# Kernel tuning notes

Hardware: AMD Instinct MI355X
Metric: run time of the kernel (lower is better)

Reference implementation:

```python
import jax, jax.numpy as jnp
import numpy as np

B, C, H, W = 8, 64, 32, 32
NEG = 256
TEMP = 2.0
FACTOR = 0.8
EPS = 1e-8


def setup_inputs() -> dict:
    key = jax.random.key(0)
    k1, k2, k3, k4 = jax.random.split(key, 4)
    views_1 = jax.random.normal(k1, (B, C, H, W), dtype=jnp.float32)
    views_2 = jax.random.normal(k2, (B, C, H, W), dtype=jnp.float32)
    img = jax.random.uniform(k3, (1, 3, H, W), dtype=jnp.float32)
    neg_idx = jax.random.randint(k4, (B, 2, H * W, NEG), 0, H, dtype=jnp.int32)
    return {"views_1": views_1, "views_2": views_2, "img": img, "neg_idx": neg_idx}


def _forward(views_1, views_2, img, neg_idx):
    hw = H * W
    height = jnp.arange(hw) // W
    width = jnp.arange(hw) % W
    coords = jnp.stack([height, width]).astype(jnp.float32)  # [2, hw]
    img0 = img[0]  # [3, H, W]; original uses img[0] for EVERY batch element
    euc_norm = jnp.sqrt(jnp.asarray((H - 1) ** 2 + (W - 1) ** 2, jnp.float32))
    sqrt3 = jnp.sqrt(jnp.asarray(3.0, jnp.float32))

    center = img0[:, height, width]  # [3, hw]

    def per_sample(z1, z2, nidx):
        # nidx: [2, hw, neg]
        nf = nidx.astype(jnp.float32)
        # torch.norm with no dim => scalar Frobenius norm over [2, neg] per pixel
        d = coords[:, :, None] - nf  # [2, hw, neg]
        euc = jnp.sqrt(jnp.sum(d * d, axis=(0, 2))) / euc_norm  # [hw]
        negs = img0[:, nidx[0], nidx[1]]  # [3, hw, neg]
        rd = center[:, :, None] - negs
        rgb = jnp.sqrt(jnp.sum(rd * rd, axis=(0, 2))) / sqrt3  # [hw]
        weight = euc * FACTOR + rgb * (1.0 - FACTOR)  # [hw], constant across neg

        z1v = z1.reshape(C, hw)  # [c, hw]
        pn = z2[:, nidx[0], nidx[1]]  # [c, hw, neg]
        dot = jnp.einsum('cp,cpn->pn', z1v, pn)  # [hw, neg]
        z1sq = jnp.sum(z1v * z1v, axis=0)  # [hw]
        z1n = jnp.sqrt(z1sq)
        pnn = jnp.sqrt(jnp.sum(pn * pn, axis=0))  # [hw, neg]
        cos = dot / jnp.maximum(z1n[:, None] * pnn, EPS)  # [hw, neg]
        cos0 = z1sq / jnp.maximum(z1sq, EPS)  # [hw] (self-similarity ~ 1)

        sim_neg = jnp.minimum(jnp.abs(cos * weight[:, None]), 1.0)  # [hw, neg]
        sim0 = jnp.minimum(jnp.abs(cos0), 1.0)  # [hw]
        sim = jnp.concatenate(
            [jnp.mean(sim0)[None], jnp.mean(sim_neg, axis=0) / TEMP]
        )  # [neg+1]

        # BCELoss with target = [1, 0, ..., 0]; torch clamps log terms at -100
        logp = jnp.maximum(jnp.log(sim[0]), -100.0)
        log1m = jnp.maximum(jnp.log1p(-sim[1:]), -100.0)
        bce = -(logp + jnp.sum(log1m)) / (NEG + 1)
        return bce, sim

    bce, sims = jax.vmap(per_sample)(views_1, views_2, neg_idx)
    loss = jnp.mean(bce)
    sim_all = jnp.sum(sims, axis=0)
    return (loss, sim_all[0] / B, jnp.sum(sim_all[1:]) / NEG * TEMP / B)


def reference(views_1, views_2, img, neg_idx):
    return _forward(views_1, views_2, img, neg_idx)
```

## Files before the change

kernel.cpp:

```cpp
#include <hip/hip_runtime.h>
#include <math.h>

#define BB 8
#define CC 64
#define HH 32
#define WW 32
#define HW 1024
#define NEGN 256
#define TEMP 2.0f
#define FACTOR 0.8f
#define EPSF 1e-8f
#define PT 8


__global__ __launch_bounds__(256) void prep(
    const float* __restrict__ z1,
    const float* __restrict__ img,
    float* __restrict__ accSim,
    float* __restrict__ accSim0,
    float* __restrict__ z1n_ws,
    float4* __restrict__ imgpack)
{
    const int b = blockIdx.x;
    const int t = threadIdx.x;

    accSim[b * NEGN + t] = 0.f;

    if (t < HW / BB) {
        const int q = b * (HW / BB) + t;
        imgpack[q] = make_float4(img[q], img[HW + q], img[2 * HW + q], 0.f);
    }

    const float4* __restrict__ z1b =
        reinterpret_cast<const float4*>(z1 + (size_t)b * CC * HW);
    float4 s = make_float4(0.f, 0.f, 0.f, 0.f);
    #pragma unroll 8
    for (int c = 0; c < CC; ++c) {
        const float4 v = z1b[c * (HW / 4) + t];
        s.x = fmaf(v.x, v.x, s.x);
        s.y = fmaf(v.y, v.y, s.y);
        s.z = fmaf(v.z, v.z, s.z);
        s.w = fmaf(v.w, v.w, s.w);
    }
    reinterpret_cast<float4*>(z1n_ws + (size_t)b * HW)[t] =
        make_float4(sqrtf(s.x), sqrtf(s.y), sqrtf(s.z), sqrtf(s.w));

    float s0 = fminf(fabsf(s.x / fmaxf(s.x, EPSF)), 1.0f)
             + fminf(fabsf(s.y / fmaxf(s.y, EPSF)), 1.0f)
             + fminf(fabsf(s.z / fmaxf(s.z, EPSF)), 1.0f)
             + fminf(fabsf(s.w / fmaxf(s.w, EPSF)), 1.0f);
    #pragma unroll
    for (int off = 32; off; off >>= 1) s0 += __shfl_down(s0, off);
    __shared__ float red[4];
    if ((t & 63) == 0) red[t >> 6] = s0;
    __syncthreads();
    if (t == 0) accSim0[b] = red[0] + red[1] + red[2] + red[3];
}

__global__ __launch_bounds__(256, 4) void contrastive_fused(
    const float* __restrict__ z1,
    const float* __restrict__ z2,
    const int*   __restrict__ nidx,
    const float* __restrict__ z1n_ws,
    const float4* __restrict__ imgpack,
    float* __restrict__ accSim)
{
    __shared__ float Dt_s[PT * HW];

    const int t  = threadIdx.x;
    const int b  = blockIdx.x >> 7;
    const int p0 = (blockIdx.x & 127) * PT;

    const int lane32 = t & 31;
    const int pp_b   = t >> 5;
    const int p_b    = p0 + pp_b;

    const float4* __restrict__ z2f4 =
        reinterpret_cast<const float4*>(z2 + (size_t)b * CC * HW);
    const float* __restrict__ z1row = z1 + (size_t)(b * CC) * HW + p0;

    float4 acc[PT];
    #pragma unroll
    for (int pp = 0; pp < PT; ++pp) acc[pp] = make_float4(0.f, 0.f, 0.f, 0.f);
    float4 sq = make_float4(0.f, 0.f, 0.f, 0.f);

    float4 pf[4];
    #pragma unroll
    for (int i = 0; i < 4; ++i) pf[i] = z2f4[i * (HW / 4) + t];

#define GEMM_STEP(kk, bv)                                                      \
    {                                                                          \
        sq.x = fmaf((bv).x, (bv).x, sq.x);                                     \
        sq.y = fmaf((bv).y, (bv).y, sq.y);                                     \
        sq.z = fmaf((bv).z, (bv).z, sq.z);                                     \
        sq.w = fmaf((bv).w, (bv).w, sq.w);                                     \
        _Pragma("unroll")                                                      \
        for (int pp = 0; pp < PT; ++pp) {                                      \
            const float a = z1row[(kk) * HW + pp];      \
            acc[pp].x = fmaf(a, (bv).x, acc[pp].x);                            \
            acc[pp].y = fmaf(a, (bv).y, acc[pp].y);                            \
            acc[pp].z = fmaf(a, (bv).z, acc[pp].z);                            \
            acc[pp].w = fmaf(a, (bv).w, acc[pp].w);                            \
        }                                                                      \
    }

    #pragma unroll 4
    for (int k = 0; k < CC - 4; ++k) {
        const float4 bv = pf[k & 3];
        pf[k & 3] = z2f4[(k + 4) * (HW / 4) + t];
        GEMM_STEP(k, bv);
    }
    #pragma unroll
    for (int k = CC - 4; k < CC; ++k) {
        const float4 bv = pf[k & 3];
        GEMM_STEP(k, bv);
    }
#undef GEMM_STEP

    const float* __restrict__ z1nrow = z1n_ws + (size_t)b * HW + p0;
    float z1nv[PT];
    #pragma unroll
    for (int pp = 0; pp < PT; ++pp) z1nv[pp] = z1nrow[pp];
    const float4 pnn = make_float4(sqrtf(sq.x), sqrtf(sq.y),
                                   sqrtf(sq.z), sqrtf(sq.w));
    float4* Dt4 = reinterpret_cast<float4*>(Dt_s);
    #pragma unroll
    for (int pp = 0; pp < PT; ++pp) {
        float4 cv;
        cv.x = acc[pp].x / fmaxf(z1nv[pp] * pnn.x, EPSF);
        cv.y = acc[pp].y / fmaxf(z1nv[pp] * pnn.y, EPSF);
        cv.z = acc[pp].z / fmaxf(z1nv[pp] * pnn.z, EPSF);
        cv.w = acc[pp].w / fmaxf(z1nv[pp] * pnn.w, EPSF);
        Dt4[pp * (HW / 4) + t] = cv;
    }

    const size_t nbase = ((size_t)(b * 2) * HW + p_b) * NEGN;
    const int2* __restrict__ nr = reinterpret_cast<const int2*>(nidx + nbase);
    const int2* __restrict__ nc =
        reinterpret_cast<const int2*>(nidx + nbase + (size_t)HW * NEGN);
    int2 rrv[4], ccv[4];
    #pragma unroll
    for (int j = 0; j < 4; ++j) {
        rrv[j] = nr[lane32 + 32 * j];
        ccv[j] = nc[lane32 + 32 * j];
    }
    __syncthreads();

    const float4 cen = imgpack[p_b];
    const float hp = (float)(p_b >> 5), wp = (float)(p_b & 31);

    int q[8];
    #pragma unroll
    for (int j = 0; j < 4; ++j) {
        q[2 * j]     = rrv[j].x * WW + ccv[j].x;
        q[2 * j + 1] = rrv[j].y * WW + ccv[j].y;
    }
    float4 g[8];
    #pragma unroll
    for (int e = 0; e < 8; ++e) g[e] = imgpack[q[e]];
    float cg[8];
    #pragma unroll
    for (int e = 0; e < 8; ++e) cg[e] = Dt_s[pp_b * HW + q[e]];

    float se = 0.f, sr = 0.f;
    #pragma unroll
    for (int j = 0; j < 4; ++j) {
        {
            const float dh = hp - (float)rrv[j].x, dw = wp - (float)ccv[j].x;
            se += dh * dh + dw * dw;
            const float d0 = cen.x - g[2 * j].x;
            const float d1 = cen.y - g[2 * j].y;
            const float d2 = cen.z - g[2 * j].z;
            sr += d0 * d0 + d1 * d1 + d2 * d2;
        }
        {
            const float dh = hp - (float)rrv[j].y, dw = wp - (float)ccv[j].y;
            se += dh * dh + dw * dw;
            const float d0 = cen.x - g[2 * j + 1].x;
            const float d1 = cen.y - g[2 * j + 1].y;
            const float d2 = cen.z - g[2 * j + 1].z;
            sr += d0 * d0 + d1 * d1 + d2 * d2;
        }
    }
    #pragma unroll
    for (int off = 16; off; off >>= 1) {
        se += __shfl_xor(se, off);
        sr += __shfl_xor(sr, off);
    }
    const float euc_norm = sqrtf((float)((HH - 1) * (HH - 1) + (WW - 1) * (WW - 1)));
    const float weight = sqrtf(se) / euc_norm * FACTOR +
                         sqrtf(sr) / sqrtf(3.0f) * (1.0f - FACTOR);

    float2 sv[4];
    #pragma unroll
    for (int j = 0; j < 4; ++j) {
        sv[j].x = fminf(fabsf(cg[2 * j]     * weight), 1.0f);
        sv[j].y = fminf(fabsf(cg[2 * j + 1] * weight), 1.0f);
    }

    __syncthreads();
    float2* simpart2 = reinterpret_cast<float2*>(Dt_s);
    #pragma unroll
    for (int j = 0; j < 4; ++j)
        simpart2[pp_b * (NEGN / 2) + lane32 + 32 * j] = sv[j];
    __syncthreads();

    float s = 0.f;
    #pragma unroll
    for (int pp = 0; pp < PT; ++pp) s += Dt_s[pp * NEGN + t];
    atomicAdd(accSim + b * NEGN + t, s);
}

__global__ __launch_bounds__(256) void finalize(
    const float* __restrict__ accSim,
    const float* __restrict__ accSim0,
    float* __restrict__ out)
{
    const int t = threadIdx.x;
    float ssum = 0.f, lsum = 0.f;
    #pragma unroll
    for (int b = 0; b < BB; ++b) {
        const float s = accSim[b * NEGN + t] * (1.0f / HW) * (1.0f / TEMP);
        ssum += s;
        lsum += fmaxf(log1pf(-s), -100.0f);
    }
    __shared__ float rs[4], rl[4];
    #pragma unroll
    for (int off = 32; off; off >>= 1) {
        ssum += __shfl_down(ssum, off);
        lsum += __shfl_down(lsum, off);
    }
    if ((t & 63) == 0) { rs[t >> 6] = ssum; rl[t >> 6] = lsum; }
    __syncthreads();

    if (t == 0) {
        const float S = rs[0] + rs[1] + rs[2] + rs[3];
        const float L = rl[0] + rl[1] + rl[2] + rl[3];
        float logpsum = 0.f, sim0sum = 0.f;
        #pragma unroll
        for (int b = 0; b < BB; ++b) {
            const float s0 = accSim0[b] * (1.0f / HW);
            sim0sum += s0;
            logpsum += fmaxf(logf(s0), -100.0f);
        }
        out[0] = -(logpsum + L) / ((float)(NEGN + 1) * (float)BB);
        out[1] = sim0sum / (float)BB;
        out[2] = S / (float)NEGN * TEMP / (float)BB;
    }
}

extern "C" void kernel_launch(void* const* d_in, const int* in_sizes, int n_in,
                              void* d_out, int out_size, void* d_ws, size_t ws_size,
                              hipStream_t stream) {
    const float* v1   = (const float*)d_in[0];
    const float* v2   = (const float*)d_in[1];
    const float* img  = (const float*)d_in[2];
    const int*   nidx = (const int*)  d_in[3];

    float* ws      = (float*)d_ws;
    float* accSim  = ws;
    float* accSim0 = accSim + BB * NEGN;
    float* z1n_ws  = accSim0 + BB;
    float4* imgpack = (float4*)(z1n_ws + BB * HW);

    prep<<<BB, 256, 0, stream>>>(v1, img, accSim, accSim0, z1n_ws, imgpack);
    contrastive_fused<<<BB * (HW / PT), 256, 0, stream>>>(
        v1, v2, nidx, z1n_ws, imgpack, accSim);
    finalize<<<1, 256, 0, stream>>>(accSim, accSim0, (float*)d_out);
}
```

Baseline: 101.1 us.

## Fold prep kernel into main kernel and replace atomics with partial-sum buffer

```diff
diff --git a/kernel.cpp b/kernel.cpp
--- a/kernel.cpp
+++ b/kernel.cpp
@@ -11,82 +11,65 @@
 #define FACTOR 0.8f
 #define EPSF 1e-8f
 #define PT 8
-
-
-__global__ __launch_bounds__(256) void prep(
-    const float* __restrict__ z1,
-    const float* __restrict__ img,
-    float* __restrict__ accSim,
-    float* __restrict__ accSim0,
-    float* __restrict__ z1n_ws,
-    float4* __restrict__ imgpack)
-{
-    const int b = blockIdx.x;
-    const int t = threadIdx.x;
-
-    accSim[b * NEGN + t] = 0.f;
-
-    if (t < HW / BB) {
-        const int q = b * (HW / BB) + t;
-        imgpack[q] = make_float4(img[q], img[HW + q], img[2 * HW + q], 0.f);
-    }
-
-    const float4* __restrict__ z1b =
-        reinterpret_cast<const float4*>(z1 + (size_t)b * CC * HW);
-    float4 s = make_float4(0.f, 0.f, 0.f, 0.f);
-    #pragma unroll 8
-    for (int c = 0; c < CC; ++c) {
-        const float4 v = z1b[c * (HW / 4) + t];
-        s.x = fmaf(v.x, v.x, s.x);
-        s.y = fmaf(v.y, v.y, s.y);
-        s.z = fmaf(v.z, v.z, s.z);
-        s.w = fmaf(v.w, v.w, s.w);
-    }
-    reinterpret_cast<float4*>(z1n_ws + (size_t)b * HW)[t] =
-        make_float4(sqrtf(s.x), sqrtf(s.y), sqrtf(s.z), sqrtf(s.w));
-
-    float s0 = fminf(fabsf(s.x / fmaxf(s.x, EPSF)), 1.0f)
-             + fminf(fabsf(s.y / fmaxf(s.y, EPSF)), 1.0f)
-             + fminf(fabsf(s.z / fmaxf(s.z, EPSF)), 1.0f)
-             + fminf(fabsf(s.w / fmaxf(s.w, EPSF)), 1.0f);
-    #pragma unroll
-    for (int off = 32; off; off >>= 1) s0 += __shfl_down(s0, off);
-    __shared__ float red[4];
-    if ((t & 63) == 0) red[t >> 6] = s0;
-    __syncthreads();
-    if (t == 0) accSim0[b] = red[0] + red[1] + red[2] + red[3];
-}
+#define RING 8
+
 
 __global__ __launch_bounds__(256, 4) void contrastive_fused(
     const float* __restrict__ z1,
     const float* __restrict__ z2,
+    const float* __restrict__ img,
     const int*   __restrict__ nidx,
-    const float* __restrict__ z1n_ws,
-    const float4* __restrict__ imgpack,
-    float* __restrict__ accSim)
+    float* __restrict__ simPart,
+    float* __restrict__ sim0Part)
 {
+    __shared__ float As_s[CC * PT];
     __shared__ float Dt_s[PT * HW];
-
-    const int t  = threadIdx.x;
-    const int b  = blockIdx.x >> 7;
-    const int p0 = (blockIdx.x & 127) * PT;
+    __shared__ float z1n_s[PT];
+    __shared__ float z1sq_s[PT];
+
+    const int t   = threadIdx.x;
+    const int blk = blockIdx.x;
+    const int b   = blk >> 7;
+    const int p0  = (blk & 127) * PT;
 
     const int lane32 = t & 31;
     const int pp_b   = t >> 5;
     const int p_b    = p0 + pp_b;
 
+    for (int i = t; i < CC * PT; i += 256) {
+        const int c = i >> 3, pp = i & 7;
+        As_s[i] = z1[((size_t)(b * CC + c)) * HW + p0 + pp];
+    }
+    __syncthreads();
+
+    {
+        const int pp = t & 7;
+        float s = 0.f;
+        #pragma unroll
+        for (int c = 0; c < CC; ++c) { const float v = As_s[c * PT + pp]; s += v * v; }
+        if (t < PT) { z1sq_s[t] = s; z1n_s[t] = sqrtf(s); }
+    }
+    __syncthreads();
+
+    if (t == 0) {
+        float s0 = 0.f;
+        #pragma unroll
+        for (int pp = 0; pp < PT; ++pp)
+            s0 += fminf(fabsf(z1sq_s[pp] / fmaxf(z1sq_s[pp], EPSF)), 1.0f);
+        sim0Part[blk] = s0;
+    }
+
     const float4* __restrict__ z2f4 =
         reinterpret_cast<const float4*>(z2 + (size_t)b * CC * HW);
-    const float* __restrict__ z1row = z1 + (size_t)(b * CC) * HW + p0;
 
     float4 acc[PT];
     #pragma unroll
     for (int pp = 0; pp < PT; ++pp) acc[pp] = make_float4(0.f, 0.f, 0.f, 0.f);
     float4 sq = make_float4(0.f, 0.f, 0.f, 0.f);
 
-    float4 pf[4];
-    #pragma unroll
-    for (int i = 0; i < 4; ++i) pf[i] = z2f4[i * (HW / 4) + t];
+    float4 pf[RING];
+    #pragma unroll
+    for (int i = 0; i < RING; ++i) pf[i] = z2f4[i * (HW / 4) + t];
 
 #define GEMM_STEP(kk, bv)                                                      \
     {                                                                          \
@@ -94,33 +77,35 @@
         sq.y = fmaf((bv).y, (bv).y, sq.y);                                     \
         sq.z = fmaf((bv).z, (bv).z, sq.z);                                     \
         sq.w = fmaf((bv).w, (bv).w, sq.w);                                     \
+        const float4 a03 = reinterpret_cast<const float4*>(As_s)[(kk) * 2];    \
+        const float4 a47 = reinterpret_cast<const float4*>(As_s)[(kk) * 2 + 1];\
+        const float av[8] = {a03.x, a03.y, a03.z, a03.w,                       \
+                             a47.x, a47.y, a47.z, a47.w};                      \
         _Pragma("unroll")                                                      \
         for (int pp = 0; pp < PT; ++pp) {                                      \
-            const float a = z1row[(kk) * HW + pp];      \
-            acc[pp].x = fmaf(a, (bv).x, acc[pp].x);                            \
-            acc[pp].y = fmaf(a, (bv).y, acc[pp].y);                            \
-            acc[pp].z = fmaf(a, (bv).z, acc[pp].z);                            \
-            acc[pp].w = fmaf(a, (bv).w, acc[pp].w);                            \
+            acc[pp].x = fmaf(av[pp], (bv).x, acc[pp].x);                       \
+            acc[pp].y = fmaf(av[pp], (bv).y, acc[pp].y);                       \
+            acc[pp].z = fmaf(av[pp], (bv).z, acc[pp].z);                       \
+            acc[pp].w = fmaf(av[pp], (bv).w, acc[pp].w);                       \
         }                                                                      \
     }
 
-    #pragma unroll 4
-    for (int k = 0; k < CC - 4; ++k) {
-        const float4 bv = pf[k & 3];
-        pf[k & 3] = z2f4[(k + 4) * (HW / 4) + t];
+    #pragma unroll 8
+    for (int k = 0; k < CC - RING; ++k) {
+        const float4 bv = pf[k & (RING - 1)];
+        pf[k & (RING - 1)] = z2f4[(k + RING) * (HW / 4) + t];
         GEMM_STEP(k, bv);
     }
     #pragma unroll
-    for (int k = CC - 4; k < CC; ++k) {
-        const float4 bv = pf[k & 3];
+    for (int k = CC - RING; k < CC; ++k) {
+        const float4 bv = pf[k & (RING - 1)];
         GEMM_STEP(k, bv);
     }
 #undef GEMM_STEP
 
-    const float* __restrict__ z1nrow = z1n_ws + (size_t)b * HW + p0;
     float z1nv[PT];
     #pragma unroll
-    for (int pp = 0; pp < PT; ++pp) z1nv[pp] = z1nrow[pp];
+    for (int pp = 0; pp < PT; ++pp) z1nv[pp] = z1n_s[pp];
     const float4 pnn = make_float4(sqrtf(sq.x), sqrtf(sq.y),
                                    sqrtf(sq.z), sqrtf(sq.w));
     float4* Dt4 = reinterpret_cast<float4*>(Dt_s);
@@ -146,7 +131,7 @@
     }
     __syncthreads();
 
-    const float4 cen = imgpack[p_b];
+    const float cen0 = img[p_b], cen1 = img[HW + p_b], cen2 = img[2 * HW + p_b];
     const float hp = (float)(p_b >> 5), wp = (float)(p_b & 31);
 
     int q[8];
@@ -155,9 +140,13 @@
         q[2 * j]     = rrv[j].x * WW + ccv[j].x;
         q[2 * j + 1] = rrv[j].y * WW + ccv[j].y;
     }
-    float4 g[8];
-    #pragma unroll
-    for (int e = 0; e < 8; ++e) g[e] = imgpack[q[e]];
+    float g0[8], g1[8], g2[8];
+    #pragma unroll
+    for (int e = 0; e < 8; ++e) {
+        g0[e] = img[q[e]];
+        g1[e] = img[HW + q[e]];
+        g2[e] = img[2 * HW + q[e]];
+    }
     float cg[8];
     #pragma unroll
     for (int e = 0; e < 8; ++e) cg[e] = Dt_s[pp_b * HW + q[e]];
@@ -168,17 +157,17 @@
         {
             const float dh = hp - (float)rrv[j].x, dw = wp - (float)ccv[j].x;
             se += dh * dh + dw * dw;
-            const float d0 = cen.x - g[2 * j].x;
-            const float d1 = cen.y - g[2 * j].y;
-            const float d2 = cen.z - g[2 * j].z;
+            const float d0 = cen0 - g0[2 * j];
+            const float d1 = cen1 - g1[2 * j];
+            const float d2 = cen2 - g2[2 * j];
             sr += d0 * d0 + d1 * d1 + d2 * d2;
         }
         {
             const float dh = hp - (float)rrv[j].y, dw = wp - (float)ccv[j].y;
             se += dh * dh + dw * dw;
-            const float d0 = cen.x - g[2 * j + 1].x;
-            const float d1 = cen.y - g[2 * j + 1].y;
-            const float d2 = cen.z - g[2 * j + 1].z;
+            const float d0 = cen0 - g0[2 * j + 1];
+            const float d1 = cen1 - g1[2 * j + 1];
+            const float d2 = cen2 - g2[2 * j + 1];
             sr += d0 * d0 + d1 * d1 + d2 * d2;
         }
     }
@@ -208,41 +197,70 @@
     float s = 0.f;
     #pragma unroll
     for (int pp = 0; pp < PT; ++pp) s += Dt_s[pp * NEGN + t];
-    atomicAdd(accSim + b * NEGN + t, s);
+    simPart[(size_t)blk * NEGN + t] = s;
 }
 
-__global__ __launch_bounds__(256) void finalize(
-    const float* __restrict__ accSim,
-    const float* __restrict__ accSim0,
+__global__ __launch_bounds__(1024) void finalize(
+    const float* __restrict__ simPart,
+    const float* __restrict__ sim0Part,
     float* __restrict__ out)
 {
+    __shared__ float part[4][BB][NEGN];
+    __shared__ float rs[4], rl[4];
+
     const int t = threadIdx.x;
+    const int quarter = t >> 8;
+    const int n = t & 255;
+
+    #pragma unroll
+    for (int b = 0; b < BB; ++b) {
+        float a = 0.f;
+        #pragma unroll 8
+        for (int i = 0; i < 32; ++i) {
+            const int pblk = quarter * 32 + i;
+            a += simPart[((size_t)(b * 128 + pblk)) * NEGN + n];
+        }
+        part[quarter][b][n] = a;
+    }
+    __syncthreads();
+
     float ssum = 0.f, lsum = 0.f;
-    #pragma unroll
-    for (int b = 0; b < BB; ++b) {
-        const float s = accSim[b * NEGN + t] * (1.0f / HW) * (1.0f / TEMP);
-        ssum += s;
-        lsum += fmaxf(log1pf(-s), -100.0f);
-    }
-    __shared__ float rs[4], rl[4];
+    if (t < 256) {
+        #pragma unroll
+        for (int b = 0; b < BB; ++b) {
+            const float sbn = part[0][b][t] + part[1][b][t] +
+                              part[2][b][t] + part[3][b][t];
+            const float s = sbn * (1.0f / HW) * (1.0f / TEMP);
+            ssum += s;
+            lsum += fmaxf(log1pf(-s), -100.0f);
+        }
+    }
     #pragma unroll
     for (int off = 32; off; off >>= 1) {
         ssum += __shfl_down(ssum, off);
         lsum += __shfl_down(lsum, off);
     }
-    if ((t & 63) == 0) { rs[t >> 6] = ssum; rl[t >> 6] = lsum; }
+    if (t < 256 && (t & 63) == 0) { rs[t >> 6] = ssum; rl[t >> 6] = lsum; }
+
+    float logpsum = 0.f, sim0sum = 0.f;
+    if (t < 64) {
+        #pragma unroll
+        for (int b = 0; b < BB; ++b) {
+            float v = sim0Part[b * 128 + t] + sim0Part[b * 128 + 64 + t];
+            #pragma unroll
+            for (int off = 32; off; off >>= 1) v += __shfl_xor(v, off);
+            if (t == 0) {
+                const float s0 = v * (1.0f / HW);
+                sim0sum += s0;
+                logpsum += fmaxf(logf(s0), -100.0f);
+            }
+        }
+    }
     __syncthreads();
 
     if (t == 0) {
         const float S = rs[0] + rs[1] + rs[2] + rs[3];
         const float L = rl[0] + rl[1] + rl[2] + rl[3];
-        float logpsum = 0.f, sim0sum = 0.f;
-        #pragma unroll
-        for (int b = 0; b < BB; ++b) {
-            const float s0 = accSim0[b] * (1.0f / HW);
-            sim0sum += s0;
-            logpsum += fmaxf(logf(s0), -100.0f);
-        }
         out[0] = -(logpsum + L) / ((float)(NEGN + 1) * (float)BB);
         out[1] = sim0sum / (float)BB;
         out[2] = S / (float)NEGN * TEMP / (float)BB;
@@ -257,14 +275,10 @@
     const float* img  = (const float*)d_in[2];
     const int*   nidx = (const int*)  d_in[3];
 
-    float* ws      = (float*)d_ws;
-    float* accSim  = ws;
-    float* accSim0 = accSim + BB * NEGN;
-    float* z1n_ws  = accSim0 + BB;
-    float4* imgpack = (float4*)(z1n_ws + BB * HW);
-
-    prep<<<BB, 256, 0, stream>>>(v1, img, accSim, accSim0, z1n_ws, imgpack);
+    float* simPart  = (float*)d_ws;
+    float* sim0Part = simPart + 1024 * NEGN;
+
     contrastive_fused<<<BB * (HW / PT), 256, 0, stream>>>(
-        v1, v2, nidx, z1n_ws, imgpack, accSim);
-    finalize<<<1, 256, 0, stream>>>(accSim, accSim0, (float*)d_out);
+        v1, v2, img, nidx, simPart, sim0Part);
+    finalize<<<1, 1024, 0, stream>>>(simPart, sim0Part, (float*)d_out);
 }
```

Result: slower. 111.1 us (+10.0%).
